# Optimization experiments

Measured on AMD Instinct MI355X. Metric: run time of the kernel, lower is better.

The kernel has to match this reference:

```python
import jax, jax.numpy as jnp
import numpy as np

B, S, HID, H = 4, 2048, 1024, 16
D = HID // H  # head_dim = 64


def setup_inputs() -> dict:
    key = jax.random.key(0)
    ks = jax.random.split(key, 12)
    std = 0.02
    inp = {
        "q": jax.random.normal(ks[0], (B, S, HID), jnp.float32),
        "k": jax.random.normal(ks[1], (B, S, HID), jnp.float32),
        "v": jax.random.normal(ks[2], (B, S, HID), jnp.float32),
        # causal mask: True where attention is NOT allowed (masked_fill semantics)
        "attn_mask": jnp.broadcast_to(
            ~jnp.tril(jnp.ones((S, S), jnp.bool_)), (B, S, S)
        ),
        "Wq": jax.random.normal(ks[3], (HID, HID), jnp.float32) * std,
        "bq": jnp.zeros((HID,), jnp.float32),
        "Wk": jax.random.normal(ks[4], (HID, HID), jnp.float32) * std,
        "bk": jnp.zeros((HID,), jnp.float32),
        "Wv": jax.random.normal(ks[5], (HID, HID), jnp.float32) * std,
        "bv": jnp.zeros((HID,), jnp.float32),
        "Wo": jax.random.normal(ks[6], (HID, HID), jnp.float32) * std,
        "bo": jnp.zeros((HID,), jnp.float32),
    }
    return inp


def _split_heads(x):
    # [B, S, HID] -> [B, H, S, D]
    b, s, _ = x.shape
    return x.reshape(b, s, H, D).transpose(0, 2, 1, 3)


def reference(q, k, v, attn_mask, Wq, bq, Wk, bk, Wv, bv, Wo, bo):
    qh = _split_heads(q @ Wq.T + bq)  # [B,H,S,D]
    kh = _split_heads(k @ Wk.T + bk)
    vh = _split_heads(v @ Wv.T + bv)
    scale = 1.0 / jnp.sqrt(jnp.asarray(D, qh.dtype))
    scores = jnp.einsum("bhqd,bhkd->bhqk", qh, kh) * scale  # [B,H,S,S]
    neg = jnp.asarray(-1e9, scores.dtype)
    scores = jnp.where(attn_mask[:, None, :, :], neg, scores)
    attn = jax.nn.softmax(scores, axis=-1)
    ctx = jnp.einsum("bhqk,bhkd->bhqd", attn, vh)  # [B,H,S,D]
    ctx = ctx.transpose(0, 2, 1, 3).reshape(q.shape[0], q.shape[1], HID)
    return ctx @ Wo.T + bo
```

## Files before the change

kernel.cpp:

```cpp
#include <hip/hip_runtime.h>

typedef __attribute__((ext_vector_type(8))) short short8;
typedef __attribute__((ext_vector_type(4))) float f32x4;
typedef __attribute__((ext_vector_type(16))) float f32x16;

#define S_LEN 2048
#define HIDN  1024
#define NHEAD 16
#define DHEAD 64

__device__ __forceinline__ short f2bf(float x) {
    unsigned u = __float_as_uint(x);
    u += 0x7fffu + ((u >> 16) & 1u);
    return (short)(u >> 16);
}

typedef const __attribute__((address_space(1))) void* gas_ptr;
typedef __attribute__((address_space(3))) void* las_ptr;

__device__ __forceinline__ void gload_lds16(const void* g, void* l) {
    __builtin_amdgcn_global_load_lds((gas_ptr)g, (las_ptr)l, 16, 0, 0);
}

__device__ __forceinline__ unsigned cvtpk(float lo, float hi_) {
    unsigned r;
    asm("v_cvt_pk_bf16_f32 %0, %1, %2" : "=v"(r) : "v"(lo), "v"(hi_));
    return r;
}

__device__ __forceinline__ void plswap(unsigned& x, unsigned& y) {
    asm("v_permlane32_swap_b32 %0, %1" : "+&v"(x), "+&v"(y));
}

__device__ __forceinline__ short8 mk8(unsigned a, unsigned b, unsigned c, unsigned d) {
    union { unsigned u[4]; short8 s; } t;
    t.u[0] = a; t.u[1] = b; t.u[2] = c; t.u[3] = d;
    return t.s;
}

__global__ __launch_bounds__(256) void cvt_all(const float* __restrict__ q,
                                               const float* __restrict__ k,
                                               const float* __restrict__ v,
                                               const float* __restrict__ Wq,
                                               const float* __restrict__ Wk,
                                               const float* __restrict__ Wv,
                                               const float* __restrict__ Wo,
                                               short* __restrict__ qb,
                                               short* __restrict__ kb,
                                               short* __restrict__ vb,
                                               short* __restrict__ wqb,
                                               short* __restrict__ wkb,
                                               short* __restrict__ wvb,
                                               short* __restrict__ wob) {
    int bid = blockIdx.x;
    const float* in;
    short* out;
    int base;
    if (bid < 2048) {
        int wsel = bid >> 9;
        base = bid & 511;
        in  = wsel == 0 ? Wq  : wsel == 1 ? Wk  : wsel == 2 ? Wv  : Wo;
        out = wsel == 0 ? wqb : wsel == 1 ? wkb : wsel == 2 ? wvb : wob;
    } else if (bid < 6144)  { in = q; out = qb; base = bid - 2048; }
    else if (bid < 10240)   { in = k; out = kb; base = bid - 6144; }
    else                    { in = v; out = vb; base = bid - 10240; }
    int i = (base * 256 + threadIdx.x) * 8;
    float4 a = *(const float4*)(in + i);
    float4 b = *(const float4*)(in + i + 4);
    short8 o;
    o[0] = f2bf(a.x); o[1] = f2bf(a.y); o[2] = f2bf(a.z); o[3] = f2bf(a.w);
    o[4] = f2bf(b.x); o[5] = f2bf(b.y); o[6] = f2bf(b.z); o[7] = f2bf(b.w);
    *(short8*)(out + i) = o;
}

__device__ __forceinline__ void gemm_k64_db8(const short* A, const short* Wb,
                                             short* As0, short* As1,
                                             short* Bs0, short* Bs1,
                                             f32x4 acc[4][2], int m0, int n0) {
    int tid = threadIdx.x;
    int w = tid >> 6, l = tid & 63, g = l >> 4, r = l & 15;
    int wm = w >> 2, wn = w & 3;
    int r7 = r & 7;

    int s0 = w * 64 + l, s1 = s0 + 512;
    int row0 = s0 >> 3, src0 = (((s0 & 7) ^ (row0 & 7))) * 8;
    int row1 = s1 >> 3, src1 = (((s1 & 7) ^ (row1 & 7))) * 8;
    int d0 = s0 * 8, d1 = s1 * 8;

    gload_lds16(A + (size_t)(m0 + row0) * HIDN + src0, As0 + d0);
    gload_lds16(A + (size_t)(m0 + row1) * HIDN + src1, As0 + d1);
    gload_lds16(Wb + (size_t)(n0 + row0) * HIDN + src0, Bs0 + d0);
    gload_lds16(Wb + (size_t)(n0 + row1) * HIDN + src1, Bs0 + d1);
    __syncthreads();

    for (int kt = 0; kt < HIDN / 64; ++kt) {
        short* Asc = (kt & 1) ? As1 : As0;
        short* Bsc = (kt & 1) ? Bs1 : Bs0;
        short* Asn = (kt & 1) ? As0 : As1;
        short* Bsn = (kt & 1) ? Bs0 : Bs1;
        if (kt + 1 < HIDN / 64) {
            int kc = (kt + 1) * 64;
            gload_lds16(A + (size_t)(m0 + row0) * HIDN + kc + src0, Asn + d0);
            gload_lds16(A + (size_t)(m0 + row1) * HIDN + kc + src1, Asn + d1);
            gload_lds16(Wb + (size_t)(n0 + row0) * HIDN + kc + src0, Bsn + d0);
            gload_lds16(Wb + (size_t)(n0 + row1) * HIDN + kc + src1, Bsn + d1);
        }
        short8 af[4][2], bfr[2][2];
#pragma unroll
        for (int i = 0; i < 4; i++)
#pragma unroll
            for (int ks = 0; ks < 2; ks++)
                af[i][ks] = *(const short8*)(Asc + (wm * 64 + i * 16 + r) * 64 +
                                             ((((ks << 2) + g) ^ r7) << 3));
#pragma unroll
        for (int j = 0; j < 2; j++)
#pragma unroll
            for (int ks = 0; ks < 2; ks++)
                bfr[j][ks] = *(const short8*)(Bsc + (wn * 32 + j * 16 + r) * 64 +
                                              ((((ks << 2) + g) ^ r7) << 3));
        __builtin_amdgcn_s_setprio(1);
#pragma unroll
        for (int i = 0; i < 4; i++)
#pragma unroll
            for (int j = 0; j < 2; j++) {
                acc[i][j] = __builtin_amdgcn_mfma_f32_16x16x32_bf16(af[i][0], bfr[j][0], acc[i][j], 0, 0, 0);
                acc[i][j] = __builtin_amdgcn_mfma_f32_16x16x32_bf16(af[i][1], bfr[j][1], acc[i][j], 0, 0, 0);
            }
        __builtin_amdgcn_s_setprio(0);
        __syncthreads();
    }
}

__global__ __launch_bounds__(512) void gemm_qkv(const short* __restrict__ qb,
                                                const short* __restrict__ kb,
                                                const short* __restrict__ vb,
                                                const short* __restrict__ Wqb,
                                                const short* __restrict__ Wkb,
                                                const short* __restrict__ Wvb,
                                                const float* __restrict__ bq,
                                                const float* __restrict__ bk,
                                                const float* __restrict__ bv,
                                                short* __restrict__ Qh,
                                                short* __restrict__ Kh,
                                                short* __restrict__ VhT,
                                                float qscale) {
    int which = blockIdx.x >> 9;
    int bid = blockIdx.x & 511;
    const short* A = which == 0 ? qb : which == 1 ? kb : vb;
    const short* Wb = which == 0 ? Wqb : which == 1 ? Wkb : Wvb;
    const float* bias = which == 0 ? bq : which == 1 ? bk : bv;
    short* Out = which == 0 ? Qh : which == 1 ? Kh : VhT;
    float oscale = which == 0 ? qscale : 1.0f;
    int omode = which == 2 ? 1 : 0;

    int mt = bid & 63, nt = bid >> 6;
    int m0 = mt * 128, n0 = nt * 128;
    int tid = threadIdx.x;
    int w = tid >> 6, l = tid & 63, g = l >> 4, r = l & 15;
    int wm = w >> 2, wn = w & 3;

    __shared__ short As0[128 * 64], As1[128 * 64];
    __shared__ short Bs0[128 * 64], Bs1[128 * 64];

    f32x4 acc[4][2];
#pragma unroll
    for (int i = 0; i < 4; i++)
#pragma unroll
        for (int j = 0; j < 2; j++) acc[i][j] = (f32x4){0.f, 0.f, 0.f, 0.f};

    gemm_k64_db8(A, Wb, As0, As1, Bs0, Bs1, acc, m0, n0);

#pragma unroll
    for (int j = 0; j < 2; j++) {
        int n_g = n0 + wn * 32 + j * 16 + r;
        float bv2 = bias[n_g];
        int h = n_g >> 6, d = n_g & 63;
#pragma unroll
        for (int i = 0; i < 4; i++) {
#pragma unroll
            for (int rr = 0; rr < 4; rr++) {
                int m_g = m0 + wm * 64 + i * 16 + g * 4 + rr;
                float val = (acc[i][j][rr] + bv2) * oscale;
                int b = m_g >> 11, s = m_g & 2047;
                size_t idx = (omode == 0)
                    ? (((size_t)(b * NHEAD + h)) * S_LEN + s) * DHEAD + d
                    : (((size_t)(b * NHEAD + h)) * DHEAD + d) * S_LEN + s;
                Out[idx] = f2bf(val);
            }
        }
    }
}

__global__ __launch_bounds__(512) void gemm_out(const short* __restrict__ A,
                                                const short* __restrict__ Wb,
                                                const float* __restrict__ bias,
                                                float* __restrict__ Out) {
    int mt = blockIdx.x & 63, nt = blockIdx.x >> 6;
    int m0 = mt * 128, n0 = nt * 128;
    int tid = threadIdx.x;
    int w = tid >> 6, l = tid & 63, g = l >> 4, r = l & 15;
    int wm = w >> 2, wn = w & 3;

    __shared__ short As0[128 * 64], As1[128 * 64];
    __shared__ short Bs0[128 * 64], Bs1[128 * 64];

    f32x4 acc[4][2];
#pragma unroll
    for (int i = 0; i < 4; i++)
#pragma unroll
        for (int j = 0; j < 2; j++) acc[i][j] = (f32x4){0.f, 0.f, 0.f, 0.f};

    gemm_k64_db8(A, Wb, As0, As1, Bs0, Bs1, acc, m0, n0);

#pragma unroll
    for (int j = 0; j < 2; j++) {
        int n_g = n0 + wn * 32 + j * 16 + r;
        float bv = bias[n_g];
#pragma unroll
        for (int i = 0; i < 4; i++) {
#pragma unroll
            for (int rr = 0; rr < 4; rr++) {
                int m_g = m0 + wm * 64 + i * 16 + g * 4 + rr;
                Out[(size_t)m_g * HIDN + n_g] = acc[i][j][rr] + bv;
            }
        }
    }
}

__global__ __launch_bounds__(512) void attn_kernel(const short* __restrict__ Qh,
                                                   const short* __restrict__ Kh,
                                                   const short* __restrict__ VhT,
                                                   short* __restrict__ ctx) {
    int bid = blockIdx.x;
    int m = bid >> 8;
    int u = bid & 255;
    int q4 = u >> 6;
    int bh = ((u >> 3) & 7) * 8 + (u & 7);
    int qt = (m == 0) ? q4 : (m == 1) ? (7 - q4) : (m == 2) ? (8 + q4) : (15 - q4);
    int tid = threadIdx.x;
    int w = tid >> 6, l = tid & 63;
    int ql = l & 31, hi = l >> 5;
    int wq = w & 3, grp = w >> 2;

    __align__(16) __shared__ char smem[34816];
    short* KVb = (short*)smem + grp * 8192;
    float* MG = (float*)smem;

    const short* Qb = Qh + (size_t)bh * (S_LEN * DHEAD);
    const short* Kb = Kh + (size_t)bh * (S_LEN * DHEAD);
    const short* Vb = VhT + (size_t)bh * (DHEAD * S_LEN);

    int h = qt + 1;
    int base = grp ? h : 0;

    int tc = tid & 255;
    int srow0 = tc >> 3, srow1 = srow0 + 32;
    int scol = (tc & 7) * 8;
    int wo0 = srow0 * 64 + (scol ^ ((srow0 & 7) << 3));
    int wo1 = srow1 * 64 + (scol ^ ((srow1 & 7) << 3));

    int r0 = ql, r1 = 32 + ql;
    int sw = (ql & 7) << 3;
    int ch = hi * 8;
    int b = bh >> 4, hd = bh & 15;

    int q_g = qt * 128 + wq * 32 + ql;
    const short* qp = Qb + (size_t)q_g * DHEAD + hi * 8;
    short8 qf0 = *(const short8*)(qp);
    short8 qf1 = *(const short8*)(qp + 16);
    short8 qf2 = *(const short8*)(qp + 32);
    short8 qf3 = *(const short8*)(qp + 48);

    f32x16 accA, accB;
#pragma unroll
    for (int i = 0; i < 16; ++i) { accA[i] = 0.f; accB[i] = 0.f; }
    float lrun = 0.f;

    int ktp = (qt * 128 + wq * 32) >> 6;

    short8 pk0 = *(const short8*)(Kb + (size_t)base * 64 * DHEAD + srow0 * 64 + scol);
    short8 pk1 = *(const short8*)(Kb + (size_t)base * 64 * DHEAD + srow1 * 64 + scol);
    short8 pv0 = *(const short8*)(Vb + (size_t)srow0 * S_LEN + base * 64 + scol);
    short8 pv1 = *(const short8*)(Vb + (size_t)srow1 * S_LEN + base * 64 + scol);

    for (int it = 0; it < h; ++it) {
        __syncthreads();
        *(short8*)(KVb + wo0) = pk0;
        *(short8*)(KVb + wo1) = pk1;
        *(short8*)(KVb + 4096 + wo0) = pv0;
        *(short8*)(KVb + 4096 + wo1) = pv1;
        __syncthreads();
        int g = base + it;
        if (it + 1 < h) {
            int gn = g + 1;
            pk0 = *(const short8*)(Kb + (size_t)gn * 64 * DHEAD + srow0 * 64 + scol);
            pk1 = *(const short8*)(Kb + (size_t)gn * 64 * DHEAD + srow1 * 64 + scol);
            pv0 = *(const short8*)(Vb + (size_t)srow0 * S_LEN + gn * 64 + scol);
            pv1 = *(const short8*)(Vb + (size_t)srow1 * S_LEN + gn * 64 + scol);
        }
        if (g <= ktp) {
            const short* Ksb = KVb;
            const short* Vsb = KVb + 4096;
            f32x16 st0, st1;
#pragma unroll
            for (int i = 0; i < 16; ++i) { st0[i] = 0.f; st1[i] = 0.f; }
            {
                short8 kA, kB;
                kA = *(const short8*)(Ksb + r0 * 64 + ((0 + ch) ^ sw));
                kB = *(const short8*)(Ksb + r1 * 64 + ((0 + ch) ^ sw));
                __builtin_amdgcn_s_setprio(1);
                st0 = __builtin_amdgcn_mfma_f32_32x32x16_bf16(kA, qf0, st0, 0, 0, 0);
                st1 = __builtin_amdgcn_mfma_f32_32x32x16_bf16(kB, qf0, st1, 0, 0, 0);
                __builtin_amdgcn_s_setprio(0);
                kA = *(const short8*)(Ksb + r0 * 64 + ((16 + ch) ^ sw));
                kB = *(const short8*)(Ksb + r1 * 64 + ((16 + ch) ^ sw));
                __builtin_amdgcn_s_setprio(1);
                st0 = __builtin_amdgcn_mfma_f32_32x32x16_bf16(kA, qf1, st0, 0, 0, 0);
                st1 = __builtin_amdgcn_mfma_f32_32x32x16_bf16(kB, qf1, st1, 0, 0, 0);
                __builtin_amdgcn_s_setprio(0);
                kA = *(const short8*)(Ksb + r0 * 64 + ((32 + ch) ^ sw));
                kB = *(const short8*)(Ksb + r1 * 64 + ((32 + ch) ^ sw));
                __builtin_amdgcn_s_setprio(1);
                st0 = __builtin_amdgcn_mfma_f32_32x32x16_bf16(kA, qf2, st0, 0, 0, 0);
                st1 = __builtin_amdgcn_mfma_f32_32x32x16_bf16(kB, qf2, st1, 0, 0, 0);
                __builtin_amdgcn_s_setprio(0);
                kA = *(const short8*)(Ksb + r0 * 64 + ((48 + ch) ^ sw));
                kB = *(const short8*)(Ksb + r1 * 64 + ((48 + ch) ^ sw));
                __builtin_amdgcn_s_setprio(1);
                st0 = __builtin_amdgcn_mfma_f32_32x32x16_bf16(kA, qf3, st0, 0, 0, 0);
                st1 = __builtin_amdgcn_mfma_f32_32x32x16_bf16(kB, qf3, st1, 0, 0, 0);
                __builtin_amdgcn_s_setprio(0);
            }
            float p[32];
#pragma unroll
            for (int i = 0; i < 16; ++i) { p[i] = st0[i]; p[16 + i] = st1[i]; }
            if (g == ktp) {
#pragma unroll
                for (int i = 0; i < 32; ++i) {
                    int kl = (i & 3) + 8 * ((i >> 2) & 3) + 32 * (i >> 4) + 4 * hi;
                    if (g * 64 + kl > q_g) p[i] = -1e30f;
                }
            }
#pragma unroll
            for (int i = 0; i < 32; ++i) p[i] = exp2f(p[i]);
            float t[16];
#pragma unroll
            for (int i = 0; i < 16; ++i) t[i] = p[i] + p[i + 16];
#pragma unroll
            for (int i = 0; i < 8; ++i) t[i] = t[i] + t[i + 8];
#pragma unroll
            for (int i = 0; i < 4; ++i) t[i] = t[i] + t[i + 4];
            float rs = (t[0] + t[1]) + (t[2] + t[3]);
            rs += __shfl_xor(rs, 32);
            lrun += rs;
            {
                unsigned u0 = cvtpk(p[0], p[1]);
                unsigned u1 = cvtpk(p[2], p[3]);
                unsigned u2 = cvtpk(p[4], p[5]);
                unsigned u3 = cvtpk(p[6], p[7]);
                plswap(u0, u2);
                plswap(u1, u3);
                short8 pfA = mk8(u0, u1, u2, u3);
                unsigned u4 = cvtpk(p[8], p[9]);
                unsigned u5 = cvtpk(p[10], p[11]);
                unsigned u6 = cvtpk(p[12], p[13]);
                unsigned u7 = cvtpk(p[14], p[15]);
                plswap(u4, u6);
                plswap(u5, u7);
                short8 pfB = mk8(u4, u5, u6, u7);
                short8 vA0 = *(const short8*)(Vsb + r0 * 64 + ((0 + ch) ^ sw));
                short8 vB0 = *(const short8*)(Vsb + r1 * 64 + ((0 + ch) ^ sw));
                short8 vA1 = *(const short8*)(Vsb + r0 * 64 + ((16 + ch) ^ sw));
                short8 vB1 = *(const short8*)(Vsb + r1 * 64 + ((16 + ch) ^ sw));
                __builtin_amdgcn_s_setprio(1);
                accA = __builtin_amdgcn_mfma_f32_32x32x16_bf16(vA0, pfA, accA, 0, 0, 0);
                accB = __builtin_amdgcn_mfma_f32_32x32x16_bf16(vB0, pfA, accB, 0, 0, 0);
                accA = __builtin_amdgcn_mfma_f32_32x32x16_bf16(vA1, pfB, accA, 0, 0, 0);
                accB = __builtin_amdgcn_mfma_f32_32x32x16_bf16(vB1, pfB, accB, 0, 0, 0);
                __builtin_amdgcn_s_setprio(0);
            }
            {
                unsigned u0 = cvtpk(p[16], p[17]);
                unsigned u1 = cvtpk(p[18], p[19]);
                unsigned u2 = cvtpk(p[20], p[21]);
                unsigned u3 = cvtpk(p[22], p[23]);
                plswap(u0, u2);
                plswap(u1, u3);
                short8 pfC = mk8(u0, u1, u2, u3);
                unsigned u4 = cvtpk(p[24], p[25]);
                unsigned u5 = cvtpk(p[26], p[27]);
                unsigned u6 = cvtpk(p[28], p[29]);
                unsigned u7 = cvtpk(p[30], p[31]);
                plswap(u4, u6);
                plswap(u5, u7);
                short8 pfD = mk8(u4, u5, u6, u7);
                short8 vA2 = *(const short8*)(Vsb + r0 * 64 + ((32 + ch) ^ sw));
                short8 vB2 = *(const short8*)(Vsb + r1 * 64 + ((32 + ch) ^ sw));
                short8 vA3 = *(const short8*)(Vsb + r0 * 64 + ((48 + ch) ^ sw));
                short8 vB3 = *(const short8*)(Vsb + r1 * 64 + ((48 + ch) ^ sw));
                __builtin_amdgcn_s_setprio(1);
                accA = __builtin_amdgcn_mfma_f32_32x32x16_bf16(vA2, pfC, accA, 0, 0, 0);
                accB = __builtin_amdgcn_mfma_f32_32x32x16_bf16(vB2, pfC, accB, 0, 0, 0);
                accA = __builtin_amdgcn_mfma_f32_32x32x16_bf16(vA3, pfD, accA, 0, 0, 0);
                accB = __builtin_amdgcn_mfma_f32_32x32x16_bf16(vB3, pfD, accB, 0, 0, 0);
                __builtin_amdgcn_s_setprio(0);
            }
        }
    }

    __syncthreads();
    if (grp == 1) {
        float* mg = MG + ((wq << 6) + l) * 34;
#pragma unroll
        for (int i = 0; i < 16; ++i) { mg[i] = accA[i]; mg[16 + i] = accB[i]; }
        mg[32] = lrun;
    }
    __syncthreads();
    if (grp == 0) {
        float* mg = MG + ((wq << 6) + l) * 34;
#pragma unroll
        for (int i = 0; i < 16; ++i) { accA[i] += mg[i]; accB[i] += mg[16 + i]; }
        lrun += mg[32];
        float inv = 1.0f / lrun;
        short* cb = ctx + ((size_t)(b * S_LEN + q_g)) * HIDN + hd * DHEAD;
#pragma unroll
        for (int i = 0; i < 16; ++i) {
            int d0 = (i & 3) + 8 * (i >> 2) + 4 * hi;
            cb[d0] = f2bf(accA[i] * inv);
            cb[32 + d0] = f2bf(accB[i] * inv);
        }
    }
}

extern "C" void kernel_launch(void* const* d_in, const int* in_sizes, int n_in,
                              void* d_out, int out_size, void* d_ws, size_t ws_size,
                              hipStream_t stream) {
    const float* q  = (const float*)d_in[0];
    const float* k  = (const float*)d_in[1];
    const float* v  = (const float*)d_in[2];
    const float* Wq = (const float*)d_in[4];
    const float* bq = (const float*)d_in[5];
    const float* Wk = (const float*)d_in[6];
    const float* bk = (const float*)d_in[7];
    const float* Wv = (const float*)d_in[8];
    const float* bv = (const float*)d_in[9];
    const float* Wo = (const float*)d_in[10];
    const float* bo = (const float*)d_in[11];

    char* ws = (char*)d_ws;
    const size_t ACT = (size_t)8192 * 1024 * 2;
    const size_t WSZ = (size_t)1024 * 1024 * 2;
    short* Qh  = (short*)(ws);
    short* Kh  = (short*)(ws + ACT);
    short* VhT = (short*)(ws + 2 * ACT);
    short* qb  = (short*)(ws + 3 * ACT);
    short* kb  = (short*)(ws + 4 * ACT);
    short* vb  = (short*)(ws + 5 * ACT);
    short* ctx = qb;
    short* Wqb = (short*)(ws + 6 * ACT);
    short* Wkb = (short*)(ws + 6 * ACT + WSZ);
    short* Wvb = (short*)(ws + 6 * ACT + 2 * WSZ);
    short* Wob = (short*)(ws + 6 * ACT + 3 * WSZ);

    cvt_all<<<14336, 256, 0, stream>>>(q, k, v, Wq, Wk, Wv, Wo,
                                       qb, kb, vb, Wqb, Wkb, Wvb, Wob);

    const float QSCALE = 0.125f * 1.44269504088896340736f;
    gemm_qkv<<<1536, 512, 0, stream>>>(qb, kb, vb, Wqb, Wkb, Wvb, bq, bk, bv,
                                       Qh, Kh, VhT, QSCALE);

    attn_kernel<<<1024, 512, 0, stream>>>(Qh, Kh, VhT, ctx);

    gemm_out<<<512, 512, 0, stream>>>(ctx, Wob, bo, (float*)d_out);
}
```

Measured before the change: 194.2 us.

## Pair short and long causal query tiles per block with double-buffered KV

Each attention block now handles two query tiles, j and 15-j, so every block does the same number of causal KV steps: 17 iterations, with the warp groups splitting the work. The grid drops from 1024 to 512 blocks. KV staging moves to a double-buffered LDS layout, so the next tile's store happens after compute and only one barrier is needed per iteration. The goal is to remove load imbalance across causal tiles and halve the barrier count. In exchange it doubles LDS use, fixes the iteration count, and adds a mid-loop switch of the query tile in group 0.

```diff
diff --git a/kernel.cpp b/kernel.cpp
--- a/kernel.cpp
+++ b/kernel.cpp
@@ -232,26 +232,23 @@
                                                    const short* __restrict__ VhT,
                                                    short* __restrict__ ctx) {
     int bid = blockIdx.x;
-    int m = bid >> 8;
-    int u = bid & 255;
-    int q4 = u >> 6;
-    int bh = ((u >> 3) & 7) * 8 + (u & 7);
-    int qt = (m == 0) ? q4 : (m == 1) ? (7 - q4) : (m == 2) ? (8 + q4) : (15 - q4);
+    int j = bid >> 6;
+    int bh = ((bid >> 3) & 7) * 8 + (bid & 7);
     int tid = threadIdx.x;
     int w = tid >> 6, l = tid & 63;
     int ql = l & 31, hi = l >> 5;
     int wq = w & 3, grp = w >> 2;
 
-    __align__(16) __shared__ char smem[34816];
-    short* KVb = (short*)smem + grp * 8192;
-    float* MG = (float*)smem;
+    __shared__ short KV[2][2][8192];
+    float* MG = (float*)&KV[0][0][0];
 
     const short* Qb = Qh + (size_t)bh * (S_LEN * DHEAD);
     const short* Kb = Kh + (size_t)bh * (S_LEN * DHEAD);
     const short* Vb = VhT + (size_t)bh * (DHEAD * S_LEN);
 
-    int h = qt + 1;
-    int base = grp ? h : 0;
+    int qtS = j, qtL = 15 - j;
+    int swpt = 2 * j + 2;
+    int qt = grp ? qtL : qtS;
 
     int tc = tid & 255;
     int srow0 = tc >> 3, srow1 = srow0 + 32;
@@ -262,7 +259,7 @@
     int r0 = ql, r1 = 32 + ql;
     int sw = (ql & 7) << 3;
     int ch = hi * 8;
-    int b = bh >> 4, hd = bh & 15;
+    int b = bh >> 4, h = bh & 15;
 
     int q_g = qt * 128 + wq * 32 + ql;
     const short* qp = Qb + (size_t)q_g * DHEAD + hi * 8;
@@ -276,31 +273,59 @@
     for (int i = 0; i < 16; ++i) { accA[i] = 0.f; accB[i] = 0.f; }
     float lrun = 0.f;
 
-    int ktp = (qt * 128 + wq * 32) >> 6;
-
-    short8 pk0 = *(const short8*)(Kb + (size_t)base * 64 * DHEAD + srow0 * 64 + scol);
-    short8 pk1 = *(const short8*)(Kb + (size_t)base * 64 * DHEAD + srow1 * 64 + scol);
-    short8 pv0 = *(const short8*)(Vb + (size_t)srow0 * S_LEN + base * 64 + scol);
-    short8 pv1 = *(const short8*)(Vb + (size_t)srow1 * S_LEN + base * 64 + scol);
-
-    for (int it = 0; it < h; ++it) {
+    int ktp = 2 * qt + (wq >> 1);
+
+    {
+        short8 k0 = *(const short8*)(Kb + srow0 * 64 + scol);
+        short8 k1 = *(const short8*)(Kb + srow1 * 64 + scol);
+        short8 v0 = *(const short8*)(Vb + (size_t)srow0 * S_LEN + scol);
+        short8 v1 = *(const short8*)(Vb + (size_t)srow1 * S_LEN + scol);
+        *(short8*)(&KV[grp][0][wo0]) = k0;
+        *(short8*)(&KV[grp][0][wo1]) = k1;
+        *(short8*)(&KV[grp][0][4096 + wo0]) = v0;
+        *(short8*)(&KV[grp][0][4096 + wo1]) = v1;
+    }
+
+    for (int it = 0; it < 17; ++it) {
         __syncthreads();
-        *(short8*)(KVb + wo0) = pk0;
-        *(short8*)(KVb + wo1) = pk1;
-        *(short8*)(KVb + 4096 + wo0) = pv0;
-        *(short8*)(KVb + 4096 + wo1) = pv1;
-        __syncthreads();
-        int g = base + it;
-        if (it + 1 < h) {
-            int gn = g + 1;
-            pk0 = *(const short8*)(Kb + (size_t)gn * 64 * DHEAD + srow0 * 64 + scol);
-            pk1 = *(const short8*)(Kb + (size_t)gn * 64 * DHEAD + srow1 * 64 + scol);
-            pv0 = *(const short8*)(Vb + (size_t)srow0 * S_LEN + gn * 64 + scol);
-            pv1 = *(const short8*)(Vb + (size_t)srow1 * S_LEN + gn * 64 + scol);
-        }
+        int cur = it & 1;
+        short8 pk0, pk1, pv0, pv1;
+        bool pf = (it + 1 < 17);
+        if (pf) {
+            int itn = it + 1;
+            int gs = grp ? itn : (itn < swpt ? itn : itn + 15 - 2 * j);
+            const short* Kt = Kb + (size_t)gs * (64 * DHEAD);
+            const short* Vt = Vb + gs * 64;
+            pk0 = *(const short8*)(Kt + srow0 * 64 + scol);
+            pk1 = *(const short8*)(Kt + srow1 * 64 + scol);
+            pv0 = *(const short8*)(Vt + (size_t)srow0 * S_LEN + scol);
+            pv1 = *(const short8*)(Vt + (size_t)srow1 * S_LEN + scol);
+        }
+        if (!grp && it == swpt) {
+            float inv = 1.0f / lrun;
+            short* cb = ctx + ((size_t)(b * S_LEN + q_g)) * HIDN + h * DHEAD;
+#pragma unroll
+            for (int i = 0; i < 16; ++i) {
+                int d0 = (i & 3) + 8 * (i >> 2) + 4 * hi;
+                cb[d0] = f2bf(accA[i] * inv);
+                cb[32 + d0] = f2bf(accB[i] * inv);
+            }
+            qt = qtL;
+            q_g = qt * 128 + wq * 32 + ql;
+            const short* qp2 = Qb + (size_t)q_g * DHEAD + hi * 8;
+            qf0 = *(const short8*)(qp2);
+            qf1 = *(const short8*)(qp2 + 16);
+            qf2 = *(const short8*)(qp2 + 32);
+            qf3 = *(const short8*)(qp2 + 48);
+            ktp = 2 * qt + (wq >> 1);
+#pragma unroll
+            for (int i = 0; i < 16; ++i) { accA[i] = 0.f; accB[i] = 0.f; }
+            lrun = 0.f;
+        }
+        int g = grp ? it : (it < swpt ? it : it + 15 - 2 * j);
         if (g <= ktp) {
-            const short* Ksb = KVb;
-            const short* Vsb = KVb + 4096;
+            const short* Ksb = &KV[grp][cur][0];
+            const short* Vsb = &KV[grp][cur][4096];
             f32x16 st0, st1;
 #pragma unroll
             for (int i = 0; i < 16; ++i) { st0[i] = 0.f; st1[i] = 0.f; }
@@ -406,23 +431,30 @@
                 __builtin_amdgcn_s_setprio(0);
             }
         }
+        if (pf) {
+            int nb = (it + 1) & 1;
+            *(short8*)(&KV[grp][nb][wo0]) = pk0;
+            *(short8*)(&KV[grp][nb][wo1]) = pk1;
+            *(short8*)(&KV[grp][nb][4096 + wo0]) = pv0;
+            *(short8*)(&KV[grp][nb][4096 + wo1]) = pv1;
+        }
     }
 
     __syncthreads();
     if (grp == 1) {
-        float* mg = MG + ((wq << 6) + l) * 34;
+        float* mg = MG + ((wq << 6) + l) * 33;
 #pragma unroll
         for (int i = 0; i < 16; ++i) { mg[i] = accA[i]; mg[16 + i] = accB[i]; }
         mg[32] = lrun;
     }
     __syncthreads();
     if (grp == 0) {
-        float* mg = MG + ((wq << 6) + l) * 34;
+        float* mg = MG + ((wq << 6) + l) * 33;
 #pragma unroll
         for (int i = 0; i < 16; ++i) { accA[i] += mg[i]; accB[i] += mg[16 + i]; }
         lrun += mg[32];
         float inv = 1.0f / lrun;
-        short* cb = ctx + ((size_t)(b * S_LEN + q_g)) * HIDN + hd * DHEAD;
+        short* cb = ctx + ((size_t)(b * S_LEN + q_g)) * HIDN + h * DHEAD;
 #pragma unroll
         for (int i = 0; i < 16; ++i) {
             int d0 = (i & 3) + 8 * (i >> 2) + 4 * hi;
@@ -469,7 +501,7 @@
     gemm_qkv<<<1536, 512, 0, stream>>>(qb, kb, vb, Wqb, Wkb, Wvb, bq, bk, bv,
                                        Qh, Kh, VhT, QSCALE);
 
-    attn_kernel<<<1024, 512, 0, stream>>>(Qh, Kh, VhT, ctx);
+    attn_kernel<<<512, 512, 0, stream>>>(Qh, Kh, VhT, ctx);
 
     gemm_out<<<512, 512, 0, stream>>>(ctx, Wob, bo, (float*)d_out);
 }
```

Result: no change. 195.6 us (+0.7%).
